# Optimization experiments

Hardware: AMD Instinct MI355X
Metric: run time of the kernel (lower is better)

## Reference

```python
import jax, jax.numpy as jnp
import numpy as np

B, S, E, H = 2, 2048, 1024, 16
DH = E // H  # 64
FF = 4 * E


def setup_inputs() -> dict:
    key = jax.random.key(0)
    ks = jax.random.split(key, 13)
    s = 0.02
    return {
        "x": jax.random.normal(ks[0], (B, S, E), dtype=jnp.float32),
        "Wq": jax.random.normal(ks[1], (H, E, DH), dtype=jnp.float32) * s,
        "Wk": jax.random.normal(ks[2], (H, E, DH), dtype=jnp.float32) * s,
        "Wv": jax.random.normal(ks[3], (H, E, DH), dtype=jnp.float32) * s,
        "Wo": jax.random.normal(ks[4], (E, E), dtype=jnp.float32) * s,
        "bo": jnp.zeros((E,), dtype=jnp.float32),
        "W1": jax.random.normal(ks[5], (E, FF), dtype=jnp.float32) * s,
        "b1": jnp.zeros((FF,), dtype=jnp.float32),
        "W2": jax.random.normal(ks[6], (FF, E), dtype=jnp.float32) * s,
        "b2": jnp.zeros((E,), dtype=jnp.float32),
        "g1": jnp.ones((E,), dtype=jnp.float32),
        "beta1": jnp.zeros((E,), dtype=jnp.float32),
        "g2": jnp.ones((E,), dtype=jnp.float32),
        "beta2": jnp.zeros((E,), dtype=jnp.float32),
    }


def _layernorm(x, g, b, eps=1e-5):
    mu = jnp.mean(x, axis=-1, keepdims=True)
    var = jnp.var(x, axis=-1, keepdims=True)
    return (x - mu) * jax.lax.rsqrt(var + eps) * g + b


def reference(x, Wq, Wk, Wv, Wo, bo, W1, b1, W2, b2, g1, beta1, g2, beta2):
    # Pre-LN attention (dropout is identity in eval mode)
    nx = _layernorm(x, g1, beta1)
    # per-head projections, batched over heads: [B,H,S,DH]
    q = jnp.einsum('bse,hed->bhsd', nx, Wq)
    k = jnp.einsum('bse,hed->bhsd', nx, Wk)
    v = jnp.einsum('bse,hed->bhsd', nx, Wv)
    scores = jnp.einsum('bhqd,bhkd->bhqk', q, k) * (DH ** -0.5)  # [B,H,S,S]
    seq = x.shape[1]
    causal = jnp.tril(jnp.ones((seq, seq), dtype=bool))
    scores = jnp.where(causal, scores, -jnp.inf)
    w = jax.nn.softmax(scores, axis=-1)
    attn = jnp.einsum('bhqk,bhkd->bhqd', w, v)  # [B,H,S,DH]
    # concat heads (head order matches ModuleList cat order)
    attn = attn.transpose(0, 2, 1, 3).reshape(x.shape[0], seq, E)
    attn_out = attn @ Wo + bo
    x = x + attn_out
    # FFN
    nx2 = _layernorm(x, g2, beta2)
    ffn = jax.nn.relu(nx2 @ W1 + b1) @ W2 + b2
    return x + ffn
```

## Files before the change

### kernel.cpp

```cpp
#include <hip/hip_runtime.h>


typedef __attribute__((ext_vector_type(8))) short short8;
typedef __attribute__((ext_vector_type(4))) float floatx4;

__device__ inline unsigned short f32_to_bf16(float f) {
  unsigned u = __float_as_uint(f);
  unsigned rb = (u >> 16) & 1u;
  u += 0x7fffu + rb;
  return (unsigned short)(u >> 16);
}
__device__ inline unsigned f32_to_bf16_hi(float f) {
  return (__float_as_uint(f) + 0x8000u) >> 16;
}
__device__ inline float bf16_to_f32(unsigned short u) {
  return __uint_as_float(((unsigned)u) << 16);
}

__global__ __launch_bounds__(256) void transpose_to_bf16(
    const float* __restrict__ in, unsigned short* __restrict__ out,
    int R, int C, int ldo, long in_bs, long out_bs) {
  __shared__ float tile[32][33];
  in  += (size_t)blockIdx.z * in_bs;
  out += (size_t)blockIdx.z * out_bs;
  const int c0 = blockIdx.x * 32, r0 = blockIdx.y * 32;
  const int tx = threadIdx.x & 31, ty = threadIdx.x >> 5;
#pragma unroll
  for (int i = 0; i < 32; i += 8)
    tile[ty + i][tx] = in[(size_t)(r0 + ty + i) * C + c0 + tx];
  __syncthreads();
#pragma unroll
  for (int i = 0; i < 32; i += 8)
    out[(size_t)(c0 + ty + i) * ldo + r0 + tx] = f32_to_bf16(tile[tx][ty + i]);
}

__global__ __launch_bounds__(256) void transpose_v(
    const unsigned short* __restrict__ qkv, unsigned short* __restrict__ vT) {
  __shared__ unsigned short tile[32][33];
  const int bh = blockIdx.z, b = bh >> 4, h = bh & 15;
  const int k0 = blockIdx.x * 32, d0 = blockIdx.y * 32;
  const int tx = threadIdx.x & 31, ty = threadIdx.x >> 5;
#pragma unroll
  for (int i = 0; i < 32; i += 8)
    tile[ty + i][tx] = qkv[(size_t)(b * 2048 + k0 + ty + i) * 3072 + 2048 + h * 64 + d0 + tx];
  __syncthreads();
#pragma unroll
  for (int i = 0; i < 32; i += 8)
    vT[((size_t)bh * 64 + d0 + ty + i) * 2048 + k0 + tx] = tile[tx][ty + i];
}

__global__ __launch_bounds__(256) void layernorm_bf16(
    const float* __restrict__ x, const float* __restrict__ g,
    const float* __restrict__ be, unsigned short* __restrict__ out) {
  const int row = blockIdx.x;
  const int t = threadIdx.x;
  floatx4 v = ((const floatx4*)(x + (size_t)row * 1024))[t];
  float s  = v[0] + v[1] + v[2] + v[3];
  float s2 = v[0]*v[0] + v[1]*v[1] + v[2]*v[2] + v[3]*v[3];
#pragma unroll
  for (int off = 1; off < 64; off <<= 1) {
    s  += __shfl_xor(s, off);
    s2 += __shfl_xor(s2, off);
  }
  __shared__ float red[8];
  const int wave = t >> 6, lane = t & 63;
  if (lane == 0) { red[wave] = s; red[wave + 4] = s2; }
  __syncthreads();
  float ts  = red[0] + red[1] + red[2] + red[3];
  float ts2 = red[4] + red[5] + red[6] + red[7];
  float mu  = ts * (1.f / 1024.f);
  float var = ts2 * (1.f / 1024.f) - mu * mu;
  float rs  = rsqrtf(var + 1e-5f);
  floatx4 gv = ((const floatx4*)g)[t];
  floatx4 bv = ((const floatx4*)be)[t];
  ushort4 ov;
  ov.x = f32_to_bf16((v[0] - mu) * rs * gv[0] + bv[0]);
  ov.y = f32_to_bf16((v[1] - mu) * rs * gv[1] + bv[1]);
  ov.z = f32_to_bf16((v[2] - mu) * rs * gv[2] + bv[2]);
  ov.w = f32_to_bf16((v[3] - mu) * rs * gv[3] + bv[3]);
  ((ushort4*)(out + (size_t)row * 1024))[t] = ov;
}

__global__ __launch_bounds__(256, 4) void gemm_bf16(
    const unsigned short* __restrict__ A, const unsigned short* __restrict__ Bt,
    const float* __restrict__ bias, const float* __restrict__ resid,
    void* __restrict__ Cout, int M, int N, int K, int mode) {
  __shared__ unsigned short As[2][4096];
  __shared__ unsigned short Bs[2][4096];
  const int t = threadIdx.x;
  const int NB = gridDim.x;
  const int bid = blockIdx.y * NB + blockIdx.x;
  const int xcd = bid & 7, slot = bid >> 3;
  const int m0 = (xcd * 4 + slot / NB) * 128;
  const int n0 = (slot % NB) * 128;
  const int lane = t & 63, wave = t >> 6;
  const int wm = (wave >> 1) * 64, wn = (wave & 1) * 64;
  const int l15 = lane & 15, quad = lane >> 4;

  floatx4 acc[4][4];
#pragma unroll
  for (int i = 0; i < 4; ++i)
#pragma unroll
    for (int j = 0; j < 4; ++j) acc[i][j] = floatx4{0.f, 0.f, 0.f, 0.f};

  const int srow = t >> 1;
  const int scol = (t & 1) * 16;
  const unsigned short* Ag = A + (size_t)(m0 + srow) * K + scol;
  const unsigned short* Bg = Bt + (size_t)(n0 + srow) * K + scol;
  const int sdst = srow * 32 + scol;

  uint4 pa0 = *(const uint4*)(Ag);
  uint4 pa1 = *(const uint4*)(Ag + 8);
  uint4 pb0 = *(const uint4*)(Bg);
  uint4 pb1 = *(const uint4*)(Bg + 8);

  const int KT = K >> 5;
  int buf = 0;
  for (int kt = 0; kt < KT; ++kt) {
    *(uint4*)&As[buf][sdst]     = pa0;
    *(uint4*)&As[buf][sdst + 8] = pa1;
    *(uint4*)&Bs[buf][sdst]     = pb0;
    *(uint4*)&Bs[buf][sdst + 8] = pb1;
    if (kt + 1 < KT) {
      const int ko = (kt + 1) * 32;
      pa0 = *(const uint4*)(Ag + ko);
      pa1 = *(const uint4*)(Ag + ko + 8);
      pb0 = *(const uint4*)(Bg + ko);
      pb1 = *(const uint4*)(Bg + ko + 8);
    }
    __syncthreads();
    short8 a[4], b[4];
#pragma unroll
    for (int i = 0; i < 4; ++i)
      a[i] = *(const short8*)&As[buf][(wm + i * 16 + l15) * 32 + quad * 8];
#pragma unroll
    for (int i = 0; i < 4; ++i)
      b[i] = *(const short8*)&Bs[buf][(wn + i * 16 + l15) * 32 + quad * 8];
#pragma unroll
    for (int i = 0; i < 4; ++i)
#pragma unroll
      for (int j = 0; j < 4; ++j)
        acc[i][j] = __builtin_amdgcn_mfma_f32_16x16x32_bf16(a[i], b[j], acc[i][j], 0, 0, 0);
    buf ^= 1;
  }

#pragma unroll
  for (int i = 0; i < 4; ++i)
#pragma unroll
    for (int j = 0; j < 4; ++j) {
      const int col = n0 + wn + j * 16 + l15;
      const int rb = m0 + wm + i * 16 + quad * 4;
#pragma unroll
      for (int r = 0; r < 4; ++r) {
        const int row = rb + r;
        float v = acc[i][j][r];
        if (mode == 0) {
          ((unsigned short*)Cout)[(size_t)row * N + col] = f32_to_bf16(v);
        } else if (mode == 1) {
          v += bias[col] + resid[(size_t)row * N + col];
          ((float*)Cout)[(size_t)row * N + col] = v;
        } else {
          v += bias[col];
          v = fmaxf(v, 0.f);
          ((unsigned short*)Cout)[(size_t)row * N + col] = f32_to_bf16(v);
        }
      }
    }
}

__global__ __launch_bounds__(256) void flash_attn_mfma(
    const unsigned short* __restrict__ qkv,
    const unsigned short* __restrict__ vT,
    unsigned short* __restrict__ attn) {
  const int b = blockIdx.z, h = blockIdx.y, bh = b * 16 + h;
  const int qt = 15 - (int)blockIdx.x;
  const int q0 = qt * 128;
  const int t = threadIdx.x;
  const int wave = t >> 6, lane = t & 63;
  const int l15 = lane & 15, quad = lane >> 4;

  __shared__ unsigned short Ks[2][64][72];
  __shared__ unsigned short Vs[2][64][72];
  __shared__ unsigned short Ps[4][32][72];

  const size_t qbase = (size_t)b * 2048 * 3072;
  const int qrow_w = q0 + wave * 32;
  const unsigned short* Kbase = qkv + qbase + 1024 + h * 64;
  const unsigned short* Vbase = vT + (size_t)bh * 64 * 2048;

  short8 qf[2][2];
#pragma unroll
  for (int mf = 0; mf < 2; ++mf)
#pragma unroll
    for (int kc = 0; kc < 2; ++kc) {
      short8 raw = *(const short8*)(qkv + qbase +
          (size_t)(qrow_w + mf * 16 + l15) * 3072 + h * 64 + kc * 32 + quad * 8);
      short8 sc;
#pragma unroll
      for (int j = 0; j < 8; ++j)
        sc[j] = (short)f32_to_bf16(bf16_to_f32((unsigned short)raw[j]) * 0.125f);
      qf[mf][kc] = sc;
    }

  floatx4 o[2][4];
  float l_s[2] = {0.f, 0.f};
#pragma unroll
  for (int mf = 0; mf < 2; ++mf)
#pragma unroll
    for (int jd = 0; jd < 4; ++jd) o[mf][jd] = floatx4{0.f, 0.f, 0.f, 0.f};

  const int sr = t >> 3, so = (t & 7) * 8;

  uint4 kr0 = *(const uint4*)(Kbase + (size_t)sr * 3072 + so);
  uint4 kr1 = *(const uint4*)(Kbase + (size_t)(sr + 32) * 3072 + so);
  uint4 vr0 = *(const uint4*)(Vbase + (size_t)sr * 2048 + so);
  uint4 vr1 = *(const uint4*)(Vbase + (size_t)(sr + 32) * 2048 + so);

  const int ntiles = 2 * qt + 2;
  int buf = 0;
  for (int kt = 0; kt < ntiles; ++kt) {
    const int k0 = kt * 64;
    *(uint4*)&Ks[buf][sr][so]      = kr0;
    *(uint4*)&Ks[buf][sr + 32][so] = kr1;
    *(uint4*)&Vs[buf][sr][so]      = vr0;
    *(uint4*)&Vs[buf][sr + 32][so] = vr1;
    if (kt + 1 < ntiles) {
      const int k1 = k0 + 64;
      kr0 = *(const uint4*)(Kbase + (size_t)(k1 + sr) * 3072 + so);
      kr1 = *(const uint4*)(Kbase + (size_t)(k1 + sr + 32) * 3072 + so);
      vr0 = *(const uint4*)(Vbase + (size_t)sr * 2048 + k1 + so);
      vr1 = *(const uint4*)(Vbase + (size_t)(sr + 32) * 2048 + k1 + so);
    }
    __syncthreads();

    if (k0 <= qrow_w + 31) {
      short8 kf[2][4];
#pragma unroll
      for (int kc = 0; kc < 2; ++kc)
#pragma unroll
        for (int jb = 0; jb < 4; ++jb)
          kf[kc][jb] = *(const short8*)&Ks[buf][jb * 16 + l15][kc * 32 + quad * 8];

      floatx4 st[2][4];
#pragma unroll
      for (int mf = 0; mf < 2; ++mf)
#pragma unroll
        for (int jb = 0; jb < 4; ++jb) st[mf][jb] = floatx4{0.f, 0.f, 0.f, 0.f};
#pragma unroll
      for (int kc = 0; kc < 2; ++kc)
#pragma unroll
        for (int jb = 0; jb < 4; ++jb) {
#pragma unroll
          for (int mf = 0; mf < 2; ++mf)
            st[mf][jb] = __builtin_amdgcn_mfma_f32_16x16x32_bf16(
                kf[kc][jb], qf[mf][kc], st[mf][jb], 0, 0, 0);
        }

#pragma unroll
      for (int mf = 0; mf < 2; ++mf) {
        const int qq = qrow_w + mf * 16 + l15;
#pragma unroll
        for (int jb = 0; jb < 4; ++jb) {
          const int keyb = k0 + jb * 16 + quad * 4;
          float p0 = (keyb + 0 > qq) ? 0.f : __expf(st[mf][jb][0]);
          float p1 = (keyb + 1 > qq) ? 0.f : __expf(st[mf][jb][1]);
          float p2 = (keyb + 2 > qq) ? 0.f : __expf(st[mf][jb][2]);
          float p3 = (keyb + 3 > qq) ? 0.f : __expf(st[mf][jb][3]);
          l_s[mf] += (p0 + p1) + (p2 + p3);
          uint2 pk;
          pk.x = (f32_to_bf16_hi(p1) << 16) | f32_to_bf16_hi(p0);
          pk.y = (f32_to_bf16_hi(p3) << 16) | f32_to_bf16_hi(p2);
          *(uint2*)&Ps[wave][mf * 16 + l15][jb * 16 + quad * 4] = pk;
        }
      }

#pragma unroll
      for (int kc = 0; kc < 2; ++kc) {
        short8 pf0 = *(const short8*)&Ps[wave][l15][kc * 32 + quad * 8];
        short8 pf1 = *(const short8*)&Ps[wave][16 + l15][kc * 32 + quad * 8];
#pragma unroll
        for (int jd = 0; jd < 4; ++jd) {
          short8 vf = *(const short8*)&Vs[buf][jd * 16 + l15][kc * 32 + quad * 8];
          o[0][jd] = __builtin_amdgcn_mfma_f32_16x16x32_bf16(pf0, vf, o[0][jd], 0, 0, 0);
          o[1][jd] = __builtin_amdgcn_mfma_f32_16x16x32_bf16(pf1, vf, o[1][jd], 0, 0, 0);
        }
      }
    }
    buf ^= 1;
  }

#pragma unroll
  for (int mf = 0; mf < 2; ++mf) {
    l_s[mf] += __shfl_xor(l_s[mf], 16);
    l_s[mf] += __shfl_xor(l_s[mf], 32);
  }

#pragma unroll
  for (int mf = 0; mf < 2; ++mf)
#pragma unroll
    for (int r = 0; r < 4; ++r) {
      const int qloc = quad * 4 + r;
      const float lsum = __shfl(l_s[mf], qloc);
      const float rl = 1.f / lsum;
      const int row = b * 2048 + q0 + wave * 32 + mf * 16 + qloc;
#pragma unroll
      for (int jd = 0; jd < 4; ++jd)
        attn[(size_t)row * 1024 + h * 64 + jd * 16 + l15] =
            f32_to_bf16(o[mf][jd][r] * rl);
    }
}

extern "C" void kernel_launch(void* const* d_in, const int* in_sizes, int n_in,
                              void* d_out, int out_size, void* d_ws, size_t ws_size,
                              hipStream_t stream) {
  const float* x   = (const float*)d_in[0];
  const float* Wq  = (const float*)d_in[1];
  const float* Wk  = (const float*)d_in[2];
  const float* Wv  = (const float*)d_in[3];
  const float* Wo  = (const float*)d_in[4];
  const float* bo  = (const float*)d_in[5];
  const float* W1  = (const float*)d_in[6];
  const float* b1  = (const float*)d_in[7];
  const float* W2  = (const float*)d_in[8];
  const float* b2  = (const float*)d_in[9];
  const float* g1  = (const float*)d_in[10];
  const float* be1 = (const float*)d_in[11];
  const float* g2  = (const float*)d_in[12];
  const float* be2 = (const float*)d_in[13];
  float* out = (float*)d_out;

  char* ws = (char*)d_ws;
  size_t off = 0;
  auto alloc = [&](size_t bytes) -> void* {
    void* p = ws + off;
    off += (bytes + 255) & ~(size_t)255;
    return p;
  };
  unsigned short* WqkvT = (unsigned short*)alloc(3072ull * 1024 * 2);
  unsigned short* WoT   = (unsigned short*)alloc(1024ull * 1024 * 2);
  unsigned short* W1T   = (unsigned short*)alloc(4096ull * 1024 * 2);
  unsigned short* W2T   = (unsigned short*)alloc(1024ull * 4096 * 2);
  unsigned short* nx    = (unsigned short*)alloc(4096ull * 1024 * 2);
  unsigned short* qkv   = (unsigned short*)alloc(4096ull * 3072 * 2);
  unsigned short* attn  = (unsigned short*)alloc(4096ull * 1024 * 2);
  float*          x1    = (float*)alloc(4096ull * 1024 * 4);
  unsigned short* nx2   = (unsigned short*)alloc(4096ull * 1024 * 2);
  unsigned short* hbuf  = (unsigned short*)alloc(4096ull * 4096 * 2);
  unsigned short* vT    = hbuf;

  dim3 blk(256);
  transpose_to_bf16<<<dim3(2, 32, 16), blk, 0, stream>>>(Wq, WqkvT, 1024, 64, 1024, 65536, 65536);
  transpose_to_bf16<<<dim3(2, 32, 16), blk, 0, stream>>>(Wk, WqkvT + 1024 * 1024, 1024, 64, 1024, 65536, 65536);
  transpose_to_bf16<<<dim3(2, 32, 16), blk, 0, stream>>>(Wv, WqkvT + 2 * 1024 * 1024, 1024, 64, 1024, 65536, 65536);
  transpose_to_bf16<<<dim3(32, 32, 1), blk, 0, stream>>>(Wo, WoT, 1024, 1024, 1024, 0, 0);
  transpose_to_bf16<<<dim3(128, 32, 1), blk, 0, stream>>>(W1, W1T, 1024, 4096, 1024, 0, 0);
  transpose_to_bf16<<<dim3(32, 128, 1), blk, 0, stream>>>(W2, W2T, 4096, 1024, 4096, 0, 0);

  layernorm_bf16<<<4096, blk, 0, stream>>>(x, g1, be1, nx);
  gemm_bf16<<<dim3(24, 32), blk, 0, stream>>>(nx, WqkvT, nullptr, nullptr, qkv, 4096, 3072, 1024, 0);
  transpose_v<<<dim3(64, 2, 32), blk, 0, stream>>>(qkv, vT);
  flash_attn_mfma<<<dim3(16, 16, 2), blk, 0, stream>>>(qkv, vT, attn);
  gemm_bf16<<<dim3(8, 32), blk, 0, stream>>>(attn, WoT, bo, x, x1, 4096, 1024, 1024, 1);
  layernorm_bf16<<<4096, blk, 0, stream>>>(x1, g2, be2, nx2);
  gemm_bf16<<<dim3(32, 32), blk, 0, stream>>>(nx2, W1T, b1, nullptr, hbuf, 4096, 4096, 1024, 2);
  gemm_bf16<<<dim3(8, 32), blk, 0, stream>>>(hbuf, W2T, b2, x1, out, 4096, 1024, 4096, 1);
}
```

Measured before the change: 415.5 us.

## Split-K the N=1024 GEMMs, pad LDS strides, and raise attention occupancy

Result: faster. 393.4 us (-5.3%).

```diff
diff --git a/kernel.cpp b/kernel.cpp
--- a/kernel.cpp
+++ b/kernel.cpp
@@ -84,15 +84,16 @@
 __global__ __launch_bounds__(256, 4) void gemm_bf16(
     const unsigned short* __restrict__ A, const unsigned short* __restrict__ Bt,
     const float* __restrict__ bias, const float* __restrict__ resid,
-    void* __restrict__ Cout, int M, int N, int K, int mode) {
-  __shared__ unsigned short As[2][4096];
-  __shared__ unsigned short Bs[2][4096];
+    void* __restrict__ Cout, int M, int N, int Kfull, int Klen, int mode) {
+  __shared__ unsigned short As[2][128 * 36];
+  __shared__ unsigned short Bs[2][128 * 36];
   const int t = threadIdx.x;
   const int NB = gridDim.x;
   const int bid = blockIdx.y * NB + blockIdx.x;
   const int xcd = bid & 7, slot = bid >> 3;
   const int m0 = (xcd * 4 + slot / NB) * 128;
   const int n0 = (slot % NB) * 128;
+  const int koff = blockIdx.z * Klen;
   const int lane = t & 63, wave = t >> 6;
   const int wm = (wave >> 1) * 64, wn = (wave & 1) * 64;
   const int l15 = lane & 15, quad = lane >> 4;
@@ -105,16 +106,16 @@
 
   const int srow = t >> 1;
   const int scol = (t & 1) * 16;
-  const unsigned short* Ag = A + (size_t)(m0 + srow) * K + scol;
-  const unsigned short* Bg = Bt + (size_t)(n0 + srow) * K + scol;
-  const int sdst = srow * 32 + scol;
+  const unsigned short* Ag = A + (size_t)(m0 + srow) * Kfull + koff + scol;
+  const unsigned short* Bg = Bt + (size_t)(n0 + srow) * Kfull + koff + scol;
+  const int sdst = srow * 36 + scol;
 
   uint4 pa0 = *(const uint4*)(Ag);
   uint4 pa1 = *(const uint4*)(Ag + 8);
   uint4 pb0 = *(const uint4*)(Bg);
   uint4 pb1 = *(const uint4*)(Bg + 8);
 
-  const int KT = K >> 5;
+  const int KT = Klen >> 5;
   int buf = 0;
   for (int kt = 0; kt < KT; ++kt) {
     *(uint4*)&As[buf][sdst]     = pa0;
@@ -132,10 +133,10 @@
     short8 a[4], b[4];
 #pragma unroll
     for (int i = 0; i < 4; ++i)
-      a[i] = *(const short8*)&As[buf][(wm + i * 16 + l15) * 32 + quad * 8];
+      a[i] = *(const short8*)&As[buf][(wm + i * 16 + l15) * 36 + quad * 8];
 #pragma unroll
     for (int i = 0; i < 4; ++i)
-      b[i] = *(const short8*)&Bs[buf][(wn + i * 16 + l15) * 32 + quad * 8];
+      b[i] = *(const short8*)&Bs[buf][(wn + i * 16 + l15) * 36 + quad * 8];
 #pragma unroll
     for (int i = 0; i < 4; ++i)
 #pragma unroll
@@ -144,6 +145,7 @@
     buf ^= 1;
   }
 
+  const size_t poff = (size_t)blockIdx.z * 4096 * 1024;
 #pragma unroll
   for (int i = 0; i < 4; ++i)
 #pragma unroll
@@ -159,16 +161,30 @@
         } else if (mode == 1) {
           v += bias[col] + resid[(size_t)row * N + col];
           ((float*)Cout)[(size_t)row * N + col] = v;
-        } else {
+        } else if (mode == 2) {
           v += bias[col];
           v = fmaxf(v, 0.f);
           ((unsigned short*)Cout)[(size_t)row * N + col] = f32_to_bf16(v);
+        } else {
+          ((float*)Cout)[poff + (size_t)row * N + col] = v;
         }
       }
     }
 }
 
-__global__ __launch_bounds__(256) void flash_attn_mfma(
+__global__ __launch_bounds__(256) void splitk_reduce(
+    const float* __restrict__ p, const float* __restrict__ bias,
+    const float* __restrict__ resid, float* __restrict__ out) {
+  const int t = threadIdx.x;
+  const size_t base = (size_t)blockIdx.x * 256 + t;
+  floatx4 a = ((const floatx4*)p)[base];
+  floatx4 b = ((const floatx4*)p)[1048576 + base];
+  floatx4 rv = ((const floatx4*)resid)[base];
+  floatx4 bv = ((const floatx4*)bias)[t];
+  ((floatx4*)out)[base] = a + b + rv + bv;
+}
+
+__global__ __launch_bounds__(256, 3) void flash_attn_mfma(
     const unsigned short* __restrict__ qkv,
     const unsigned short* __restrict__ vT,
     unsigned short* __restrict__ attn) {
@@ -179,9 +195,9 @@
   const int wave = t >> 6, lane = t & 63;
   const int l15 = lane & 15, quad = lane >> 4;
 
-  __shared__ unsigned short Ks[2][64][72];
-  __shared__ unsigned short Vs[2][64][72];
-  __shared__ unsigned short Ps[4][32][72];
+  __shared__ unsigned short Ks[2][64][68];
+  __shared__ unsigned short Vs[2][64][68];
+  __shared__ unsigned short Ps[4][32][68];
 
   const size_t qbase = (size_t)b * 2048 * 3072;
   const int qrow_w = q0 + wave * 32;
@@ -347,6 +363,7 @@
   unsigned short* nx2   = (unsigned short*)alloc(4096ull * 1024 * 2);
   unsigned short* hbuf  = (unsigned short*)alloc(4096ull * 4096 * 2);
   unsigned short* vT    = hbuf;
+  float*          part  = (float*)nx;
 
   dim3 blk(256);
   transpose_to_bf16<<<dim3(2, 32, 16), blk, 0, stream>>>(Wq, WqkvT, 1024, 64, 1024, 65536, 65536);
@@ -357,11 +374,13 @@
   transpose_to_bf16<<<dim3(32, 128, 1), blk, 0, stream>>>(W2, W2T, 4096, 1024, 4096, 0, 0);
 
   layernorm_bf16<<<4096, blk, 0, stream>>>(x, g1, be1, nx);
-  gemm_bf16<<<dim3(24, 32), blk, 0, stream>>>(nx, WqkvT, nullptr, nullptr, qkv, 4096, 3072, 1024, 0);
+  gemm_bf16<<<dim3(24, 32, 1), blk, 0, stream>>>(nx, WqkvT, nullptr, nullptr, qkv, 4096, 3072, 1024, 1024, 0);
   transpose_v<<<dim3(64, 2, 32), blk, 0, stream>>>(qkv, vT);
   flash_attn_mfma<<<dim3(16, 16, 2), blk, 0, stream>>>(qkv, vT, attn);
-  gemm_bf16<<<dim3(8, 32), blk, 0, stream>>>(attn, WoT, bo, x, x1, 4096, 1024, 1024, 1);
+  gemm_bf16<<<dim3(8, 32, 2), blk, 0, stream>>>(attn, WoT, nullptr, nullptr, part, 4096, 1024, 1024, 512, 3);
+  splitk_reduce<<<4096, blk, 0, stream>>>(part, bo, x, x1);
   layernorm_bf16<<<4096, blk, 0, stream>>>(x1, g2, be2, nx2);
-  gemm_bf16<<<dim3(32, 32), blk, 0, stream>>>(nx2, W1T, b1, nullptr, hbuf, 4096, 4096, 1024, 2);
-  gemm_bf16<<<dim3(8, 32), blk, 0, stream>>>(hbuf, W2T, b2, x1, out, 4096, 1024, 4096, 1);
-}
+  gemm_bf16<<<dim3(32, 32, 1), blk, 0, stream>>>(nx2, W1T, b1, nullptr, hbuf, 4096, 4096, 1024, 1024, 2);
+  gemm_bf16<<<dim3(8, 32, 2), blk, 0, stream>>>(hbuf, W2T, nullptr, nullptr, part, 4096, 1024, 4096, 2048, 3);
+  splitk_reduce<<<4096, blk, 0, stream>>>(part, b2, x1, out);
+}
```
